# Optimization experiments

Measured on AMD Instinct MI355X. Metric: run time of the kernel, lower is better.

Reference implementation:

```python
import jax, jax.numpy as jnp
import numpy as np

# Dims
B, S, D = 4, 4096, 1024
H, NB, A = 4, 4096, 4          # hashes, buckets, associativity
DK, DV, DT = 64, 128, 32        # key dim, value (mem) dim, vsa tag dim
BITS = 12                       # log2(NB)
TEMP = 1.0
VSA_W = 1.0
TANH_SCALE = 1.0
ETA = 0.1
WRITE_THR = 0.5
MATCH_THR = 0.0
NOV_THR = 0.0
EPS = 1e-6


def _l2n(x):
    return x / (jnp.linalg.norm(x, axis=-1, keepdims=True) + EPS)


def setup_inputs() -> dict:
    key = jax.random.key(0)
    ks = jax.random.split(key, 13)
    sc = 0.02
    return {
        "u": jax.random.normal(ks[0], (B, S, D), jnp.float32),
        "memK": jax.random.normal(ks[1], (H, NB, A, DK), jnp.float32),
        "memV": jax.random.normal(ks[2], (H, NB, A, DV), jnp.float32),
        "memT": jnp.tanh(jax.random.normal(ks[3], (H, NB, A, DT), jnp.float32)),
        "Wq": jax.random.normal(ks[4], (DK, D), jnp.float32) * sc,
        "Wwk": jax.random.normal(ks[5], (DK, D), jnp.float32) * sc,
        "Wv": jax.random.normal(ks[6], (DV, D), jnp.float32) * sc,
        "Wo": jax.random.normal(ks[7], (D, DV), jnp.float32) * sc,
        "Wg": jax.random.normal(ks[8], (1, D), jnp.float32) * sc,
        "bg": jnp.zeros((1,), jnp.float32),
        "Wvsa": jax.random.normal(ks[9], (DK, DT), jnp.float32) * sc,
        "R": jax.random.normal(ks[10], (H, DK, BITS), jnp.float32),
    }


def reference(u, memK, memV, memT, Wq, Wwk, Wv, Wo, Wg, bg, Wvsa, R):
    N = B * S
    uf = u.reshape(N, D)

    # ---- routing: sign-bit LSH over query key -> bucket index per hash ----
    qkey = uf @ Wq.T                                     # [N, DK]
    bits = (jnp.einsum("nd,hdk->nhk", qkey, R) > 0).astype(jnp.int32)
    pw = (2 ** jnp.arange(BITS, dtype=jnp.int32))
    idx = (bits * pw).sum(-1)                            # [N, H] bucket ids
    hh = jnp.arange(H)[None, :]                          # [1, H]

    # ---- associative gather read ----
    Kg = memK[hh, idx]                                   # [N, H, A, DK]
    Vg = memV[hh, idx]                                   # [N, H, A, DV]
    Tg = memT[hh, idx]                                   # [N, H, A, DT]
    qtag = jnp.tanh(TANH_SCALE * (qkey @ Wvsa))          # [N, DT]
    sc = (jnp.einsum("nd,nhad->nha", qkey, Kg) / np.sqrt(DK)
          + VSA_W * jnp.einsum("nt,nhat->nha", qtag, Tg) / np.sqrt(DT))
    w = jax.nn.softmax(sc.reshape(N, H * A) / TEMP, axis=-1)
    read = jnp.einsum("nk,nkd->nd", w, Vg.reshape(N, H * A, DV))
    y = (read @ Wo.T).reshape(B, S, D)

    # ---- gated scatter write with EMA + novelty ----
    wkey = uf @ Wwk.T                                    # [N, DK]
    wval = uf @ Wv.T                                     # [N, DV]
    gate = jax.nn.sigmoid(uf @ Wg.T + bg)                # [N, 1]
    wmask = (gate > WRITE_THR).astype(u.dtype)           # [N, 1]
    wtag = jnp.tanh(TANH_SCALE * (wkey @ Wvsa))          # [N, DT]

    sim = jnp.einsum("nd,nhad->nha", _l2n(wkey), _l2n(Kg))   # [N,H,A]
    astar = jnp.argmax(sim, axis=-1)                         # [N,H]
    bsim = jnp.max(sim, axis=-1)                             # [N,H]
    take = lambda G: jnp.take_along_axis(G, astar[:, :, None, None], axis=2)[:, :, 0]
    Kbest, Vbest, Tbest = take(Kg), take(Vg), take(Tg)       # [N,H,·]

    tagsim = jnp.einsum("nt,nhat->nha", _l2n(wtag), _l2n(Tg))
    novelty = 1.0 - jnp.max(tagsim, axis=-1)                 # [N,H]

    eff = (ETA * gate * wmask
           * (bsim >= MATCH_THR).astype(u.dtype)
           * (novelty >= NOV_THR).astype(u.dtype))           # [N,H]

    dK = eff[..., None] * (wkey[:, None, :] - Kbest)
    dV = eff[..., None] * (wval[:, None, :] - Vbest)
    dT = eff[..., None] * (wtag[:, None, :] - Tbest)
    Knew = memK.at[hh, idx, astar].add(dK)
    Vnew = memV.at[hh, idx, astar].add(dV)
    Tnew = memT.at[hh, idx, astar].add(dT)
    return y, Knew, Vnew, Tnew
```

## Files before the change

kernel.cpp:

```cpp
#include <hip/hip_runtime.h>
#include <hip/hip_bf16.h>
#include <math.h>

#define NTOK    16384
#define DMODEL  1024
#define HN      4
#define NBUCKET 4096
#define ASSOC   4
#define DKEY    64
#define DVAL    128
#define DTAG    32
#define NBITS   12
#define EPSV    1e-6f

typedef __bf16 bf16x8 __attribute__((ext_vector_type(8)));
typedef float  f32x4  __attribute__((ext_vector_type(4)));

__device__ __forceinline__ unsigned short f2bf_raw(float f) {
    __hip_bfloat16 h = __float2bfloat16(f);
    return *(unsigned short*)&h;
}

__global__ __launch_bounds__(256) void gemm_mfma(const float* __restrict__ A,
                                                 const float* __restrict__ B,
                                                 float* __restrict__ C,
                                                 int M, int N, int K) {
    __shared__ __align__(16) unsigned short As[4][128][8];
    __shared__ __align__(16) unsigned short Bs[4][128][8];
    const int t    = threadIdx.x;
    const int lane = t & 63;
    const int w    = t >> 6;
    const int wm   = (w & 1) * 64;
    const int wn   = (w >> 1) * 64;
    const int bm   = blockIdx.x * 128;
    const int bn   = blockIdx.y * 128;

    const int srow = t & 127;
    const int skg  = t >> 7;
    const float* Ap = A + (size_t)(bm + srow) * K;
    const float* Bp = B + (size_t)(bn + srow) * K;

    const int fr = lane & 15;
    const int kq = lane >> 4;

    f32x4 acc[4][4] = {};

    for (int k0 = 0; k0 < K; k0 += 32) {
        #pragma unroll
        for (int ii = 0; ii < 2; ++ii) {
            const int kg = skg + ii * 2;
            const float4 a0 = *(const float4*)(Ap + k0 + kg * 8);
            const float4 a1 = *(const float4*)(Ap + k0 + kg * 8 + 4);
            const float4 b0 = *(const float4*)(Bp + k0 + kg * 8);
            const float4 b1 = *(const float4*)(Bp + k0 + kg * 8 + 4);
            unsigned short* da = &As[kg][srow][0];
            da[0] = f2bf_raw(a0.x); da[1] = f2bf_raw(a0.y);
            da[2] = f2bf_raw(a0.z); da[3] = f2bf_raw(a0.w);
            da[4] = f2bf_raw(a1.x); da[5] = f2bf_raw(a1.y);
            da[6] = f2bf_raw(a1.z); da[7] = f2bf_raw(a1.w);
            unsigned short* db = &Bs[kg][srow][0];
            db[0] = f2bf_raw(b0.x); db[1] = f2bf_raw(b0.y);
            db[2] = f2bf_raw(b0.z); db[3] = f2bf_raw(b0.w);
            db[4] = f2bf_raw(b1.x); db[5] = f2bf_raw(b1.y);
            db[6] = f2bf_raw(b1.z); db[7] = f2bf_raw(b1.w);
        }
        __syncthreads();
        bf16x8 af[4], bfv[4];
        #pragma unroll
        for (int i = 0; i < 4; ++i) af[i]  = *(const bf16x8*)&As[kq][wm + i * 16 + fr][0];
        #pragma unroll
        for (int j = 0; j < 4; ++j) bfv[j] = *(const bf16x8*)&Bs[kq][wn + j * 16 + fr][0];
        #pragma unroll
        for (int i = 0; i < 4; ++i)
            #pragma unroll
            for (int j = 0; j < 4; ++j)
                acc[i][j] = __builtin_amdgcn_mfma_f32_16x16x32_bf16(af[i], bfv[j], acc[i][j], 0, 0, 0);
        __syncthreads();
    }
    #pragma unroll
    for (int i = 0; i < 4; ++i)
        #pragma unroll
        for (int j = 0; j < 4; ++j)
            #pragma unroll
            for (int r = 0; r < 4; ++r)
                C[(size_t)(bm + wm + i * 16 + kq * 4 + r) * N + (bn + wn + j * 16 + fr)] = acc[i][j][r];
}

__global__ __launch_bounds__(256) void gemm_mfma_n64(const float* __restrict__ A,
                                                     const float* __restrict__ B,
                                                     float* __restrict__ C,
                                                     int M, int N, int K) {
    __shared__ __align__(16) unsigned short As[4][128][8];
    __shared__ __align__(16) unsigned short Bs[4][64][8];
    const int t    = threadIdx.x;
    const int lane = t & 63;
    const int w    = t >> 6;
    const int bm   = blockIdx.x * 128;
    const int bn   = blockIdx.y * 64;

    const int srow = t & 127;
    const int skg  = t >> 7;
    const float* Ap = A + (size_t)(bm + srow) * K;
    const float* Bp = B + (size_t)(bn + (t & 63)) * K;
    const int bkg   = t >> 6;

    const int fr = lane & 15;
    const int kq = lane >> 4;

    f32x4 acc[2][4] = {};

    for (int k0 = 0; k0 < K; k0 += 32) {
        #pragma unroll
        for (int ii = 0; ii < 2; ++ii) {
            const int kg = skg + ii * 2;
            const float4 a0 = *(const float4*)(Ap + k0 + kg * 8);
            const float4 a1 = *(const float4*)(Ap + k0 + kg * 8 + 4);
            unsigned short* da = &As[kg][srow][0];
            da[0] = f2bf_raw(a0.x); da[1] = f2bf_raw(a0.y);
            da[2] = f2bf_raw(a0.z); da[3] = f2bf_raw(a0.w);
            da[4] = f2bf_raw(a1.x); da[5] = f2bf_raw(a1.y);
            da[6] = f2bf_raw(a1.z); da[7] = f2bf_raw(a1.w);
        }
        {
            const float4 b0 = *(const float4*)(Bp + k0 + bkg * 8);
            const float4 b1 = *(const float4*)(Bp + k0 + bkg * 8 + 4);
            unsigned short* db = &Bs[bkg][t & 63][0];
            db[0] = f2bf_raw(b0.x); db[1] = f2bf_raw(b0.y);
            db[2] = f2bf_raw(b0.z); db[3] = f2bf_raw(b0.w);
            db[4] = f2bf_raw(b1.x); db[5] = f2bf_raw(b1.y);
            db[6] = f2bf_raw(b1.z); db[7] = f2bf_raw(b1.w);
        }
        __syncthreads();
        bf16x8 af[2], bfv[4];
        #pragma unroll
        for (int i = 0; i < 2; ++i) af[i]  = *(const bf16x8*)&As[kq][w * 32 + i * 16 + fr][0];
        #pragma unroll
        for (int j = 0; j < 4; ++j) bfv[j] = *(const bf16x8*)&Bs[kq][j * 16 + fr][0];
        #pragma unroll
        for (int i = 0; i < 2; ++i)
            #pragma unroll
            for (int j = 0; j < 4; ++j)
                acc[i][j] = __builtin_amdgcn_mfma_f32_16x16x32_bf16(af[i], bfv[j], acc[i][j], 0, 0, 0);
        __syncthreads();
    }
    #pragma unroll
    for (int i = 0; i < 2; ++i)
        #pragma unroll
        for (int j = 0; j < 4; ++j)
            #pragma unroll
            for (int r = 0; r < 4; ++r)
                C[(size_t)(bm + w * 32 + i * 16 + kq * 4 + r) * N + (bn + j * 16 + fr)] = acc[i][j][r];
}

__global__ __launch_bounds__(256) void gemm_f32_splitk(const float* __restrict__ A,
                                                       const float* __restrict__ B,
                                                       float* __restrict__ Cpart,
                                                       int M, int K, int K_half) {
    __shared__ __align__(16) float As[16][68];
    __shared__ __align__(16) float Bs[16][136];
    const int t  = threadIdx.x;
    const int bm = blockIdx.x * 64;
    const int kz = blockIdx.z;
    const int tx = t & 15;
    const int ty = t >> 4;
    float acc[4][8] = {};
    const int arow = t >> 2, ac = (t & 3) * 4;
    const int brow = t >> 1, bc = (t & 1) * 8;
    const int kbeg = kz * K_half, kend = kbeg + K_half;
    for (int k0 = kbeg; k0 < kend; k0 += 16) {
        const float4 av = *(const float4*)(A + (size_t)(bm + arow) * K + k0 + ac);
        const float4 b0 = *(const float4*)(B + (size_t)brow * K + k0 + bc);
        const float4 b1 = *(const float4*)(B + (size_t)brow * K + k0 + bc + 4);
        As[ac + 0][arow] = av.x; As[ac + 1][arow] = av.y;
        As[ac + 2][arow] = av.z; As[ac + 3][arow] = av.w;
        Bs[bc + 0][brow] = b0.x; Bs[bc + 1][brow] = b0.y;
        Bs[bc + 2][brow] = b0.z; Bs[bc + 3][brow] = b0.w;
        Bs[bc + 4][brow] = b1.x; Bs[bc + 5][brow] = b1.y;
        Bs[bc + 6][brow] = b1.z; Bs[bc + 7][brow] = b1.w;
        __syncthreads();
        #pragma unroll
        for (int kk = 0; kk < 16; ++kk) {
            const float4 a4  = *(const float4*)&As[kk][ty * 4];
            const float4 bb0 = *(const float4*)&Bs[kk][tx * 8];
            const float4 bb1 = *(const float4*)&Bs[kk][tx * 8 + 4];
            const float a[4] = {a4.x, a4.y, a4.z, a4.w};
            const float b[8] = {bb0.x, bb0.y, bb0.z, bb0.w, bb1.x, bb1.y, bb1.z, bb1.w};
            #pragma unroll
            for (int i = 0; i < 4; ++i)
                #pragma unroll
                for (int j = 0; j < 8; ++j)
                    acc[i][j] = fmaf(a[i], b[j], acc[i][j]);
        }
        __syncthreads();
    }
    float* Cp = Cpart + (size_t)kz * M * 128;
    #pragma unroll
    for (int i = 0; i < 4; ++i)
        #pragma unroll
        for (int j = 0; j < 8; ++j)
            Cp[(size_t)(bm + ty * 4 + i) * 128 + tx * 8 + j] = acc[i][j];
}

__global__ __launch_bounds__(256) void reduce2_kernel(const float* __restrict__ p0,
                                                      const float* __restrict__ p1,
                                                      float* __restrict__ out, int n4) {
    const int i = (blockIdx.x * 256 + threadIdx.x);
    if (i < n4) {
        const float4 a = ((const float4*)p0)[i];
        const float4 b = ((const float4*)p1)[i];
        float4 r; r.x = a.x + b.x; r.y = a.y + b.y; r.z = a.z + b.z; r.w = a.w + b.w;
        ((float4*)out)[i] = r;
    }
}

__global__ __launch_bounds__(256) void gate_kernel(const float* __restrict__ u,
                                                   const float* __restrict__ Wg,
                                                   const float* __restrict__ bg,
                                                   float* __restrict__ gateg) {
    const int wv = threadIdx.x >> 6, lane = threadIdx.x & 63;
    const int n = blockIdx.x * 4 + wv;
    const float* up = u + (size_t)n * DMODEL;
    float acc = 0.f;
    #pragma unroll
    for (int j = 0; j < 16; ++j)
        acc += up[lane + 64 * j] * Wg[lane + 64 * j];
    #pragma unroll
    for (int off = 1; off < 64; off <<= 1) acc += __shfl_xor(acc, off);
    if (lane == 0) gateg[n] = 1.f / (1.f + expf(-(acc + bg[0])));
}

__global__ __launch_bounds__(256) void route_kernel(
    const float* __restrict__ memK, const float* __restrict__ memV,
    const float* __restrict__ memT, const float* __restrict__ R,
    const float* __restrict__ Wvsa,
    const float* __restrict__ qw, const float* __restrict__ wvalg,
    const float* __restrict__ gateg,
    float* __restrict__ accK, float* __restrict__ accV, float* __restrict__ accT,
    float* __restrict__ readw) {
    __shared__ float sQK[4][64], sWK[4][64], sQT[4][32], sWT[4][32];
    __shared__ float sSc[4][16], sSim[4][16], sTsim[4][16], sW[4][16];
    __shared__ int   sIdx[4][4], sAst[4][4];
    __shared__ float sEff[4][4];

    const int wv = threadIdx.x >> 6;
    const int lane = threadIdx.x & 63;
    const int n = blockIdx.x * 4 + wv;

    const float qk = qw[(size_t)n * 128 + lane];
    const float wk = qw[(size_t)n * 128 + 64 + lane];
    sQK[wv][lane] = qk;
    sWK[wv][lane] = wk;
    float wk2 = wk * wk;
    #pragma unroll
    for (int off = 1; off < 64; off <<= 1) wk2 += __shfl_xor(wk2, off);
    const float wknorm = sqrtf(wk2) + EPSV;
    __syncthreads();

    {
        const int tg = lane & 31;
        const float* keyp = (lane < 32) ? sQK[wv] : sWK[wv];
        float tacc = 0.f;
        for (int d = 0; d < 64; ++d) tacc += keyp[d] * Wvsa[d * DTAG + tg];
        const float tagv = tanhf(tacc);
        if (lane < 32) sQT[wv][tg] = tagv; else sWT[wv][tg] = tagv;
        float wt2 = (lane >= 32) ? tagv * tagv : 0.f;
        #pragma unroll
        for (int off = 1; off < 64; off <<= 1) wt2 += __shfl_xor(wt2, off);
        const float wtnorm = sqrtf(wt2) + EPSV;

        bool bit = false;
        if (lane < 48) {
            const int h = lane / 12, k = lane % 12;
            float bacc = 0.f;
            for (int d = 0; d < 64; ++d)
                bacc += sQK[wv][d] * R[(size_t)(h * DKEY + d) * NBITS + k];
            bit = bacc > 0.f;
        }
        const unsigned long long mask = __ballot(bit);
        if (lane < 4) sIdx[wv][lane] = (int)((mask >> (12 * lane)) & 0xFFFull);
        __syncthreads();

        const int slot = lane >> 2, sub = lane & 3;
        const int sh = slot >> 2, sa = slot & 3;
        const int rowS = (sh * NBUCKET + sIdx[wv][sh]) * ASSOC + sa;
        const float* Kp = memK + (size_t)rowS * DKEY;
        const float* Tp = memT + (size_t)rowS * DTAG;
        float d_qk = 0, d_wk = 0, d_kk = 0, d_qt = 0, d_wt = 0, d_tt = 0;
        for (int j = 0; j < 16; ++j) {
            const int d = sub * 16 + j;
            const float kv = Kp[d];
            d_qk += sQK[wv][d] * kv;
            d_wk += sWK[wv][d] * kv;
            d_kk += kv * kv;
        }
        for (int j = 0; j < 8; ++j) {
            const int d = sub * 8 + j;
            const float tv = Tp[d];
            d_qt += sQT[wv][d] * tv;
            d_wt += sWT[wv][d] * tv;
            d_tt += tv * tv;
        }
        #pragma unroll
        for (int off = 1; off <= 2; off <<= 1) {
            d_qk += __shfl_xor(d_qk, off);
            d_wk += __shfl_xor(d_wk, off);
            d_kk += __shfl_xor(d_kk, off);
            d_qt += __shfl_xor(d_qt, off);
            d_wt += __shfl_xor(d_wt, off);
            d_tt += __shfl_xor(d_tt, off);
        }
        if (sub == 0) {
            sSc[wv][slot]   = d_qk * 0.125f + d_qt * 0.17677669529663687f;
            sSim[wv][slot]  = d_wk / (wknorm * (sqrtf(d_kk) + EPSV));
            sTsim[wv][slot] = d_wt / (wtnorm * (sqrtf(d_tt) + EPSV));
        }
    }
    __syncthreads();

    if (lane < 16) {
        const float sc = sSc[wv][lane];
        float m = sc;
        #pragma unroll
        for (int off = 1; off < 16; off <<= 1) m = fmaxf(m, __shfl_xor(m, off, 16));
        const float e = expf(sc - m);
        float ssum = e;
        #pragma unroll
        for (int off = 1; off < 16; off <<= 1) ssum += __shfl_xor(ssum, off, 16);
        sW[wv][lane] = e / ssum;
    }
    const float gate = gateg[n];
    if (lane < 4) {
        float bs = -1e30f; int as = 0; float mt = -1e30f;
        #pragma unroll
        for (int aa = 0; aa < 4; ++aa) {
            const float sv = sSim[wv][lane * 4 + aa];
            if (sv > bs) { bs = sv; as = aa; }
            mt = fmaxf(mt, sTsim[wv][lane * 4 + aa]);
        }
        const float novelty = 1.f - mt;
        float e = 0.1f * gate;
        if (!(gate > 0.5f) || !(bs >= 0.f) || !(novelty >= 0.f)) e = 0.f;
        sEff[wv][lane] = e;
        sAst[wv][lane] = as;
    }
    __syncthreads();

    float r0 = 0.f, r1 = 0.f;
    #pragma unroll
    for (int s2 = 0; s2 < 16; ++s2) {
        const int hh = s2 >> 2, aa = s2 & 3;
        const int rw = (hh * NBUCKET + sIdx[wv][hh]) * ASSOC + aa;
        const float wgt = sW[wv][s2];
        const float* Vp = memV + (size_t)rw * DVAL;
        r0 += wgt * Vp[lane];
        r1 += wgt * Vp[64 + lane];
    }
    readw[(size_t)n * DVAL + lane]      = r0;
    readw[(size_t)n * DVAL + 64 + lane] = r1;

    const float wv0 = wvalg[(size_t)n * DVAL + lane];
    const float wv1 = wvalg[(size_t)n * DVAL + 64 + lane];
    for (int hh = 0; hh < 4; ++hh) {
        const float e = sEff[wv][hh];
        if (e == 0.f) continue;
        const int rw = (hh * NBUCKET + sIdx[wv][hh]) * ASSOC + sAst[wv][hh];
        atomicAdd(&accK[(size_t)rw * DKEY + lane],
                  e * (sWK[wv][lane] - memK[(size_t)rw * DKEY + lane]));
        atomicAdd(&accV[(size_t)rw * DVAL + lane],
                  e * (wv0 - memV[(size_t)rw * DVAL + lane]));
        atomicAdd(&accV[(size_t)rw * DVAL + 64 + lane],
                  e * (wv1 - memV[(size_t)rw * DVAL + 64 + lane]));
        if (lane < 32)
            atomicAdd(&accT[(size_t)rw * DTAG + lane],
                      e * (sWT[wv][lane] - memT[(size_t)rw * DTAG + lane]));
    }
}

extern "C" void kernel_launch(void* const* d_in, const int* in_sizes, int n_in,
                              void* d_out, int out_size, void* d_ws, size_t ws_size,
                              hipStream_t stream) {
    const float* u    = (const float*)d_in[0];
    const float* memK = (const float*)d_in[1];
    const float* memV = (const float*)d_in[2];
    const float* memT = (const float*)d_in[3];
    const float* Wq   = (const float*)d_in[4];
    const float* Wwk  = (const float*)d_in[5];
    const float* Wv   = (const float*)d_in[6];
    const float* Wo   = (const float*)d_in[7];
    const float* Wg   = (const float*)d_in[8];
    const float* bg   = (const float*)d_in[9];
    const float* Wvsa = (const float*)d_in[10];
    const float* R    = (const float*)d_in[11];

    const int nK = HN * NBUCKET * ASSOC * DKEY;
    const int nV = HN * NBUCKET * ASSOC * DVAL;
    const int nT = HN * NBUCKET * ASSOC * DTAG;

    float* y_out = (float*)d_out;
    float* K_out = y_out + (size_t)NTOK * DMODEL;
    float* V_out = K_out + nK;
    float* T_out = V_out + nV;

    float* qw    = (float*)d_ws;
    float* wvalg = qw    + (size_t)NTOK * 128;
    float* readw = wvalg + (size_t)NTOK * 128;
    float* gateg = readw + (size_t)NTOK * 128;
    float* qwW   = gateg + NTOK;

    float* part  = y_out;

    hipMemcpyAsync(qwW,          Wq,  (size_t)DKEY * DMODEL * 4, hipMemcpyDeviceToDevice, stream);
    hipMemcpyAsync(qwW + 65536,  Wwk, (size_t)DKEY * DMODEL * 4, hipMemcpyDeviceToDevice, stream);
    hipMemcpyAsync(K_out, memK, (size_t)nK * 4, hipMemcpyDeviceToDevice, stream);
    hipMemcpyAsync(V_out, memV, (size_t)nV * 4, hipMemcpyDeviceToDevice, stream);
    hipMemcpyAsync(T_out, memT, (size_t)nT * 4, hipMemcpyDeviceToDevice, stream);

    gemm_f32_splitk<<<dim3(NTOK / 64, 1, 2), 256, 0, stream>>>(u, qwW, part, NTOK, DMODEL, DMODEL / 2);
    reduce2_kernel<<<(NTOK * 128 / 4 + 255) / 256, 256, 0, stream>>>(part, part + (size_t)NTOK * 128, qw, NTOK * 128 / 4);
    gemm_mfma_n64<<<dim3(NTOK / 128, 2), 256, 0, stream>>>(u, Wv, wvalg, NTOK, DVAL, DMODEL);
    gate_kernel<<<NTOK / 4, 256, 0, stream>>>(u, Wg, bg, gateg);

    route_kernel<<<NTOK / 4, 256, 0, stream>>>(memK, memV, memT, R, Wvsa,
                                               qw, wvalg, gateg,
                                               K_out, V_out, T_out, readw);

    gemm_mfma<<<dim3(NTOK / 128, DMODEL / 128), 256, 0, stream>>>(readw, Wo, y_out, NTOK, DMODEL, DVAL);
}
```

Measured before the change: 438.4 us.

## Split-K both projection GEMMs, double-buffer fp32 GEMM with packed FMA

The fp32 query/write-key projection GEMM goes from split-K 2 to split-K 4 and gets a double-buffered LDS pipeline with register prefetch, a padded B layout, packed two-wide FMA and vectorized stores. The bf16 MFMA value projection also becomes split-K 2, followed by its own reduction. The aim is more blocks in flight for these skinny GEMMs (N=128, M=16384) and overlap of global loads with compute. In exchange there is more partial-sum traffic and extra reduction kernels, with partials staged in the y output buffer.

```diff
diff --git a/kernel.cpp b/kernel.cpp
--- a/kernel.cpp
+++ b/kernel.cpp
@@ -15,6 +15,7 @@
 
 typedef __bf16 bf16x8 __attribute__((ext_vector_type(8)));
 typedef float  f32x4  __attribute__((ext_vector_type(4)));
+typedef float  f32x2  __attribute__((ext_vector_type(2)));
 
 __device__ __forceinline__ unsigned short f2bf_raw(float f) {
     __hip_bfloat16 h = __float2bfloat16(f);
@@ -86,10 +87,10 @@
                 C[(size_t)(bm + wm + i * 16 + kq * 4 + r) * N + (bn + wn + j * 16 + fr)] = acc[i][j][r];
 }
 
-__global__ __launch_bounds__(256) void gemm_mfma_n64(const float* __restrict__ A,
-                                                     const float* __restrict__ B,
-                                                     float* __restrict__ C,
-                                                     int M, int N, int K) {
+__global__ __launch_bounds__(256) void gemm_bf16_n64_splitk(const float* __restrict__ A,
+                                                            const float* __restrict__ B,
+                                                            float* __restrict__ Cpart,
+                                                            int M, int K, int K_half) {
     __shared__ __align__(16) unsigned short As[4][128][8];
     __shared__ __align__(16) unsigned short Bs[4][64][8];
     const int t    = threadIdx.x;
@@ -97,6 +98,7 @@
     const int w    = t >> 6;
     const int bm   = blockIdx.x * 128;
     const int bn   = blockIdx.y * 64;
+    const int kz   = blockIdx.z;
 
     const int srow = t & 127;
     const int skg  = t >> 7;
@@ -109,7 +111,8 @@
 
     f32x4 acc[2][4] = {};
 
-    for (int k0 = 0; k0 < K; k0 += 32) {
+    const int kbeg = kz * K_half, kend = kbeg + K_half;
+    for (int k0 = kbeg; k0 < kend; k0 += 32) {
         #pragma unroll
         for (int ii = 0; ii < 2; ++ii) {
             const int kg = skg + ii * 2;
@@ -143,62 +146,97 @@
                 acc[i][j] = __builtin_amdgcn_mfma_f32_16x16x32_bf16(af[i], bfv[j], acc[i][j], 0, 0, 0);
         __syncthreads();
     }
+    float* Cp = Cpart + (size_t)kz * M * 128;
     #pragma unroll
     for (int i = 0; i < 2; ++i)
         #pragma unroll
         for (int j = 0; j < 4; ++j)
             #pragma unroll
             for (int r = 0; r < 4; ++r)
-                C[(size_t)(bm + w * 32 + i * 16 + kq * 4 + r) * N + (bn + j * 16 + fr)] = acc[i][j][r];
+                Cp[(size_t)(bm + w * 32 + i * 16 + kq * 4 + r) * 128 + (bn + j * 16 + fr)] = acc[i][j][r];
 }
 
 __global__ __launch_bounds__(256) void gemm_f32_splitk(const float* __restrict__ A,
                                                        const float* __restrict__ B,
                                                        float* __restrict__ Cpart,
-                                                       int M, int K, int K_half) {
-    __shared__ __align__(16) float As[16][68];
-    __shared__ __align__(16) float Bs[16][136];
+                                                       int M, int K, int K_quarter) {
+    __shared__ __align__(16) float As[2][16][68];
+    __shared__ __align__(16) float Bs[2][16][140];
     const int t  = threadIdx.x;
     const int bm = blockIdx.x * 64;
     const int kz = blockIdx.z;
     const int tx = t & 15;
     const int ty = t >> 4;
-    float acc[4][8] = {};
+
     const int arow = t >> 2, ac = (t & 3) * 4;
     const int brow = t >> 1, bc = (t & 1) * 8;
-    const int kbeg = kz * K_half, kend = kbeg + K_half;
-    for (int k0 = kbeg; k0 < kend; k0 += 16) {
-        const float4 av = *(const float4*)(A + (size_t)(bm + arow) * K + k0 + ac);
-        const float4 b0 = *(const float4*)(B + (size_t)brow * K + k0 + bc);
-        const float4 b1 = *(const float4*)(B + (size_t)brow * K + k0 + bc + 4);
-        As[ac + 0][arow] = av.x; As[ac + 1][arow] = av.y;
-        As[ac + 2][arow] = av.z; As[ac + 3][arow] = av.w;
-        Bs[bc + 0][brow] = b0.x; Bs[bc + 1][brow] = b0.y;
-        Bs[bc + 2][brow] = b0.z; Bs[bc + 3][brow] = b0.w;
-        Bs[bc + 4][brow] = b1.x; Bs[bc + 5][brow] = b1.y;
-        Bs[bc + 6][brow] = b1.z; Bs[bc + 7][brow] = b1.w;
-        __syncthreads();
+    const int bperm = brow + ((brow >> 5) << 2);
+    const int goff  = tx * 8 + ((tx >> 2) << 2);
+
+    const float* Apt = A + (size_t)(bm + arow) * K + ac;
+    const float* Bpt = B + (size_t)brow * K + bc;
+
+    const int kbeg = kz * K_quarter;
+    const int NSTEP = 16;
+
+    f32x2 acc2[4][4] = {};
+
+    float4 av = *(const float4*)(Apt + kbeg);
+    float4 b0 = *(const float4*)(Bpt + kbeg);
+    float4 b1 = *(const float4*)(Bpt + kbeg + 4);
+    As[0][ac + 0][arow] = av.x; As[0][ac + 1][arow] = av.y;
+    As[0][ac + 2][arow] = av.z; As[0][ac + 3][arow] = av.w;
+    Bs[0][bc + 0][bperm] = b0.x; Bs[0][bc + 1][bperm] = b0.y;
+    Bs[0][bc + 2][bperm] = b0.z; Bs[0][bc + 3][bperm] = b0.w;
+    Bs[0][bc + 4][bperm] = b1.x; Bs[0][bc + 5][bperm] = b1.y;
+    Bs[0][bc + 6][bperm] = b1.z; Bs[0][bc + 7][bperm] = b1.w;
+    __syncthreads();
+
+    for (int s = 0; s < NSTEP; ++s) {
+        const int cur = s & 1;
+        if (s + 1 < NSTEP) {
+            const int k0 = kbeg + (s + 1) * 16;
+            av = *(const float4*)(Apt + k0);
+            b0 = *(const float4*)(Bpt + k0);
+            b1 = *(const float4*)(Bpt + k0 + 4);
+        }
         #pragma unroll
         for (int kk = 0; kk < 16; ++kk) {
-            const float4 a4  = *(const float4*)&As[kk][ty * 4];
-            const float4 bb0 = *(const float4*)&Bs[kk][tx * 8];
-            const float4 bb1 = *(const float4*)&Bs[kk][tx * 8 + 4];
-            const float a[4] = {a4.x, a4.y, a4.z, a4.w};
-            const float b[8] = {bb0.x, bb0.y, bb0.z, bb0.w, bb1.x, bb1.y, bb1.z, bb1.w};
+            const float4 a4 = *(const float4*)&As[cur][kk][ty * 4];
+            const float4 v0 = *(const float4*)&Bs[cur][kk][goff];
+            const float4 v1 = *(const float4*)&Bs[cur][kk][goff + 4];
+            const float aa[4] = {a4.x, a4.y, a4.z, a4.w};
+            const f32x2 bb[4] = {{v0.x, v0.y}, {v0.z, v0.w}, {v1.x, v1.y}, {v1.z, v1.w}};
             #pragma unroll
-            for (int i = 0; i < 4; ++i)
+            for (int i = 0; i < 4; ++i) {
+                const f32x2 as2 = {aa[i], aa[i]};
                 #pragma unroll
-                for (int j = 0; j < 8; ++j)
-                    acc[i][j] = fmaf(a[i], b[j], acc[i][j]);
-        }
-        __syncthreads();
-    }
+                for (int j = 0; j < 4; ++j)
+                    acc2[i][j] = __builtin_elementwise_fma(as2, bb[j], acc2[i][j]);
+            }
+        }
+        if (s + 1 < NSTEP) {
+            const int nb = cur ^ 1;
+            As[nb][ac + 0][arow] = av.x; As[nb][ac + 1][arow] = av.y;
+            As[nb][ac + 2][arow] = av.z; As[nb][ac + 3][arow] = av.w;
+            Bs[nb][bc + 0][bperm] = b0.x; Bs[nb][bc + 1][bperm] = b0.y;
+            Bs[nb][bc + 2][bperm] = b0.z; Bs[nb][bc + 3][bperm] = b0.w;
+            Bs[nb][bc + 4][bperm] = b1.x; Bs[nb][bc + 5][bperm] = b1.y;
+            Bs[nb][bc + 6][bperm] = b1.z; Bs[nb][bc + 7][bperm] = b1.w;
+        }
+        __syncthreads();
+    }
+
     float* Cp = Cpart + (size_t)kz * M * 128;
     #pragma unroll
-    for (int i = 0; i < 4; ++i)
-        #pragma unroll
-        for (int j = 0; j < 8; ++j)
-            Cp[(size_t)(bm + ty * 4 + i) * 128 + tx * 8 + j] = acc[i][j];
+    for (int i = 0; i < 4; ++i) {
+        float4 o0, o1;
+        o0.x = acc2[i][0].x; o0.y = acc2[i][0].y; o0.z = acc2[i][1].x; o0.w = acc2[i][1].y;
+        o1.x = acc2[i][2].x; o1.y = acc2[i][2].y; o1.z = acc2[i][3].x; o1.w = acc2[i][3].y;
+        float* dst = &Cp[(size_t)(bm + ty * 4 + i) * 128 + tx * 8];
+        *(float4*)dst       = o0;
+        *(float4*)(dst + 4) = o1;
+    }
 }
 
 __global__ __launch_bounds__(256) void reduce2_kernel(const float* __restrict__ p0,
@@ -209,6 +247,24 @@
         const float4 a = ((const float4*)p0)[i];
         const float4 b = ((const float4*)p1)[i];
         float4 r; r.x = a.x + b.x; r.y = a.y + b.y; r.z = a.z + b.z; r.w = a.w + b.w;
+        ((float4*)out)[i] = r;
+    }
+}
+
+__global__ __launch_bounds__(256) void reduce4_kernel(const float* __restrict__ p,
+                                                      float* __restrict__ out,
+                                                      int n4, int stride4) {
+    const int i = (blockIdx.x * 256 + threadIdx.x);
+    if (i < n4) {
+        const float4 a = ((const float4*)p)[i];
+        const float4 b = ((const float4*)p)[i + stride4];
+        const float4 c = ((const float4*)p)[i + 2 * stride4];
+        const float4 d = ((const float4*)p)[i + 3 * stride4];
+        float4 r;
+        r.x = (a.x + b.x) + (c.x + d.x);
+        r.y = (a.y + b.y) + (c.y + d.y);
+        r.z = (a.z + b.z) + (c.z + d.z);
+        r.w = (a.w + b.w) + (c.w + d.w);
         ((float4*)out)[i] = r;
     }
 }
@@ -408,6 +464,7 @@
     float* qwW   = gateg + NTOK;
 
     float* part  = y_out;
+    float* part2 = y_out + (size_t)4 * NTOK * 128;
 
     hipMemcpyAsync(qwW,          Wq,  (size_t)DKEY * DMODEL * 4, hipMemcpyDeviceToDevice, stream);
     hipMemcpyAsync(qwW + 65536,  Wwk, (size_t)DKEY * DMODEL * 4, hipMemcpyDeviceToDevice, stream);
@@ -415,9 +472,10 @@
     hipMemcpyAsync(V_out, memV, (size_t)nV * 4, hipMemcpyDeviceToDevice, stream);
     hipMemcpyAsync(T_out, memT, (size_t)nT * 4, hipMemcpyDeviceToDevice, stream);
 
-    gemm_f32_splitk<<<dim3(NTOK / 64, 1, 2), 256, 0, stream>>>(u, qwW, part, NTOK, DMODEL, DMODEL / 2);
-    reduce2_kernel<<<(NTOK * 128 / 4 + 255) / 256, 256, 0, stream>>>(part, part + (size_t)NTOK * 128, qw, NTOK * 128 / 4);
-    gemm_mfma_n64<<<dim3(NTOK / 128, 2), 256, 0, stream>>>(u, Wv, wvalg, NTOK, DVAL, DMODEL);
+    gemm_f32_splitk<<<dim3(NTOK / 64, 1, 4), 256, 0, stream>>>(u, qwW, part, NTOK, DMODEL, DMODEL / 4);
+    reduce4_kernel<<<(NTOK * 128 / 4 + 255) / 256, 256, 0, stream>>>(part, qw, NTOK * 128 / 4, NTOK * 128 / 4);
+    gemm_bf16_n64_splitk<<<dim3(NTOK / 128, 2, 2), 256, 0, stream>>>(u, Wv, part2, NTOK, DMODEL, DMODEL / 2);
+    reduce2_kernel<<<(NTOK * 128 / 4 + 255) / 256, 256, 0, stream>>>(part2, part2 + (size_t)NTOK * 128, wvalg, NTOK * 128 / 4);
     gate_kernel<<<NTOK / 4, 256, 0, stream>>>(u, Wg, bg, gateg);
 
     route_kernel<<<NTOK / 4, 256, 0, stream>>>(memK, memV, memT, R, Wvsa,
```

Result: faster. 420.4 us (-4.1%).
